# Kernel tuning notes

Measured on AMD Instinct MI355X. Metric: run time of the kernel, lower is better.

The kernel has to match this reference:

```python
import jax, jax.numpy as jnp
import numpy as np

B, K, D, L, POS = 128, 128, 512, 2, 64
DI = 2 * D           # d_inner = dim * expand(2)
HH, WW = 64, 64
GS = 16              # hilbert grid_size


def _ln(x, g, b):
    m = jnp.mean(x, axis=-1, keepdims=True)
    v = jnp.mean(jnp.square(x - m), axis=-1, keepdims=True)
    return (x - m) * jax.lax.rsqrt(v + 1e-5) * g + b


def _ssm(x, g, b, wi, bi, wo, bo):
    # LinearAttentionSSM: x + proj_out(silu(z) * sigmoid(gate)) with z,gate = proj_in(LN(x)).chunk(2)
    h = _ln(x, g, b) @ wi + bi
    z, gate = jnp.split(h, 2, axis=-1)
    return x + (jax.nn.silu(z) * jax.nn.sigmoid(gate)) @ wo + bo


def _hilbert_d(x, y, n=GS):
    # vectorized xy2d_hilbert over arbitrary int arrays
    d = jnp.zeros_like(x)
    s = n // 2
    while s > 0:
        rx = ((x & s) > 0).astype(jnp.int32)
        ry = ((y & s) > 0).astype(jnp.int32)
        d = d + s * s * jnp.bitwise_xor(3 * rx, ry)
        x, y = (jnp.where(ry == 0, jnp.where(rx == 1, s - 1 - y, y), x),
                jnp.where(ry == 0, jnp.where(rx == 1, s - 1 - x, x), y))
        s //= 2
    return d


def _forward(H, W, slots, keep_mask, attn_maps,
             pm1_w, pm1_b, pm2_w, pm2_b,
             fwd_ln_g, fwd_ln_b, fwd_in_w, fwd_in_b, fwd_out_w, fwd_out_b,
             bwd_ln_g, bwd_ln_b, bwd_in_w, bwd_in_b, bwd_out_w, bwd_out_b,
             merge_w, merge_b, norm_g, norm_b,
             ffn_ln_g, ffn_ln_b, ffn1_w, ffn1_b, ffn2_w, ffn2_b):
    Bz, Kz, Dz = slots.shape
    dt = slots.dtype
    # ---- SlotSpatialEncoder ----
    gy = jnp.arange(H, dtype=dt) / max(H - 1, 1)
    gx = jnp.arange(W, dtype=dt) / max(W - 1, 1)
    grid_y, grid_x = jnp.meshgrid(gy, gx, indexing='ij')
    coords = jnp.stack([grid_x.ravel(), grid_y.ravel()], axis=-1)       # [N,2]
    ap = attn_maps[:, :Kz, :]
    ap = ap / (ap.sum(axis=-1, keepdims=True) + 1e-8)
    centroids = jnp.einsum('bkn,nc->bkc', ap, coords)                   # [B,K,2]
    feats = jnp.concatenate([centroids, jnp.full_like(centroids, 0.1)], axis=-1)  # [B,K,4]
    freqs = 1.0 / (10000.0 ** (jnp.arange(0, POS, 2, dtype=jnp.float32) / POS))
    angles = feats[..., None] * freqs * 3.14159                         # [B,K,4,POS//2]
    enc = jnp.concatenate([jnp.sin(angles), jnp.cos(angles)], axis=-1).reshape(Bz, Kz, 4 * POS)
    pos_enc = jax.nn.gelu(enc @ pm1_w + pm1_b, approximate=False) @ pm2_w + pm2_b
    slots = slots + pos_enc
    # ---- Hilbert ordering (same centroids => same order each layer) ----
    cx = jnp.clip(centroids[..., 0] * (GS - 1), 0, GS - 1).astype(jnp.int32)
    cy = jnp.clip(centroids[..., 1] * (GS - 1), 0, GS - 1).astype(jnp.int32)
    order = jnp.argsort(_hilbert_d(cx, cy), axis=-1)                    # [B,K]
    reverse = jnp.argsort(order, axis=-1)
    # ---- layers ----
    for i in range(L):
        residual = slots
        ordered = jnp.take_along_axis(slots, order[..., None], axis=1)
        f = _ssm(ordered, fwd_ln_g[i], fwd_ln_b[i], fwd_in_w[i], fwd_in_b[i], fwd_out_w[i], fwd_out_b[i])
        bk = _ssm(ordered[:, ::-1], bwd_ln_g[i], bwd_ln_b[i], bwd_in_w[i], bwd_in_b[i], bwd_out_w[i], bwd_out_b[i])[:, ::-1]
        merged = jnp.concatenate([f, bk], axis=-1) @ merge_w[i] + merge_b[i]
        unord = jnp.take_along_axis(merged, reverse[..., None], axis=1)
        slots = _ln(residual + unord, norm_g[i], norm_b[i])
        ff = jax.nn.gelu(_ln(slots, ffn_ln_g[i], ffn_ln_b[i]) @ ffn1_w[i] + ffn1_b[i], approximate=False) @ ffn2_w[i] + ffn2_b[i]
        slots = slots + ff
        slots = slots * keep_mask[..., None]
    return slots, centroids


def setup_inputs() -> dict:
    key = jax.random.key(0)
    ks = iter(jax.random.split(key, 32))
    w = lambda *s: jax.random.normal(next(ks), s, jnp.float32) * 0.02
    z = lambda *s: jnp.zeros(s, jnp.float32)
    o = lambda *s: jnp.ones(s, jnp.float32)
    return {
        'slots': jax.random.normal(next(ks), (B, K, D), jnp.float32),
        'keep_mask': o(B, K),
        'attn_maps': jax.random.uniform(next(ks), (B, K, HH * WW), jnp.float32),
        'H': HH, 'W': WW,
        'pm1_w': w(4 * POS, D), 'pm1_b': z(D), 'pm2_w': w(D, D), 'pm2_b': z(D),
        'fwd_ln_g': o(L, D), 'fwd_ln_b': z(L, D),
        'fwd_in_w': w(L, D, 2 * DI), 'fwd_in_b': z(L, 2 * DI),
        'fwd_out_w': w(L, DI, D), 'fwd_out_b': z(L, D),
        'bwd_ln_g': o(L, D), 'bwd_ln_b': z(L, D),
        'bwd_in_w': w(L, D, 2 * DI), 'bwd_in_b': z(L, 2 * DI),
        'bwd_out_w': w(L, DI, D), 'bwd_out_b': z(L, D),
        'merge_w': w(L, 2 * D, D), 'merge_b': z(L, D),
        'norm_g': o(L, D), 'norm_b': z(L, D),
        'ffn_ln_g': o(L, D), 'ffn_ln_b': z(L, D),
        'ffn1_w': w(L, D, 4 * D), 'ffn1_b': z(L, 4 * D),
        'ffn2_w': w(L, 4 * D, D), 'ffn2_b': z(L, D),
    }


def reference(slots, keep_mask, attn_maps, H, W,
              pm1_w, pm1_b, pm2_w, pm2_b,
              fwd_ln_g, fwd_ln_b, fwd_in_w, fwd_in_b, fwd_out_w, fwd_out_b,
              bwd_ln_g, bwd_ln_b, bwd_in_w, bwd_in_b, bwd_out_w, bwd_out_b,
              merge_w, merge_b, norm_g, norm_b,
              ffn_ln_g, ffn_ln_b, ffn1_w, ffn1_b, ffn2_w, ffn2_b):
    return _forward(H, W, slots, keep_mask, attn_maps,
                    pm1_w, pm1_b, pm2_w, pm2_b,
                    fwd_ln_g, fwd_ln_b, fwd_in_w, fwd_in_b, fwd_out_w, fwd_out_b,
                    bwd_ln_g, bwd_ln_b, bwd_in_w, bwd_in_b, bwd_out_w, bwd_out_b,
                    merge_w, merge_b, norm_g, norm_b,
                    ffn_ln_g, ffn_ln_b, ffn1_w, ffn1_b, ffn2_w, ffn2_b)
```

## Files before the change

kernel.cpp:

```cpp
#include <hip/hip_runtime.h>

typedef __bf16 bf16_t;
typedef __bf16 bf16x8 __attribute__((ext_vector_type(8)));
typedef __bf16 bf16x4 __attribute__((ext_vector_type(4)));
typedef float  f32x4  __attribute__((ext_vector_type(4)));

#define MODE_GELU   0
#define MODE_GATED  1
#define MODE_RES_BF 2
#define MODE_RES_F  3
#define MODE_FFN2   4

__device__ __forceinline__ void async16(const void* g, void* l) {
  __builtin_amdgcn_global_load_lds(
      (const __attribute__((address_space(1))) void*)g,
      (__attribute__((address_space(3))) void*)l, 16, 0, 0);
}

__device__ __forceinline__ float fast_exp(float x) {
  return __builtin_amdgcn_exp2f(x * 1.44269504088896f);
}
__device__ __forceinline__ float fast_sigmoid(float x) {
  return __builtin_amdgcn_rcpf(1.0f + fast_exp(-x));
}
__device__ __forceinline__ float fast_gelu(float x) {
  float u = fabsf(x) * 0.70710678118f;
  float t = __builtin_amdgcn_rcpf(fmaf(0.3275911f, u, 1.0f));
  float p = t * fmaf(t, fmaf(t, fmaf(t, fmaf(t, 1.061405429f, -1.453152027f),
                                     1.421413741f), -0.284496736f), 0.254829592f);
  float e = __builtin_amdgcn_exp2f(-u * u * 1.44269504088896f);
  float erfu = fmaf(-p, e, 1.0f);
  float s = (x >= 0.f) ? erfu : -erfu;
  return 0.5f * x * (1.0f + s);
}

template<int MODE>
__launch_bounds__(256, 2)
__global__ void gemm_mfma(const bf16_t* __restrict__ A,
                          const bf16_t* __restrict__ B1,
                          const bf16_t* __restrict__ B2,
                          const float*  __restrict__ bias,
                          const float*  __restrict__ Xres,
                          const float*  __restrict__ mask,
                          void* __restrict__ Cptr,
                          int M, int N, int K, int ldC, int coff)
{
  constexpr bool DUAL = (MODE == MODE_GATED);
  __shared__ bf16_t sA[128 * 64];
  __shared__ bf16_t sB[128 * 64];
  __shared__ bf16_t sB2[DUAL ? 128 * 64 : 8];

  const int tid  = threadIdx.x;
  const int wave = tid >> 6;
  const int lane = tid & 63;
  const int wm = wave & 1;
  const int wn = wave >> 1;
  const long m0 = (long)blockIdx.y * 128;
  const long n0 = (long)blockIdx.x * 128;

  f32x4 zero4 = {0.f, 0.f, 0.f, 0.f};
  f32x4 acc[4][4];
  f32x4 acc2[DUAL ? 4 : 1][DUAL ? 4 : 1];
#pragma unroll
  for (int i = 0; i < 4; i++)
#pragma unroll
    for (int j = 0; j < 4; j++) acc[i][j] = zero4;
  if constexpr (DUAL) {
#pragma unroll
    for (int i = 0; i < 4; i++)
#pragma unroll
      for (int j = 0; j < 4; j++) acc2[i][j] = zero4;
  }

  const int q    = lane >> 4;
  const int c16  = lane & 15;
  const int sr   = lane >> 3;
  const int sg   = lane & 7;
  const int stRow = wave * 8 + sr;

  for (long k0 = 0; k0 < K; k0 += 64) {
#pragma unroll
    for (int i = 0; i < 4; i++) {
      int  r     = i * 32 + stRow;
      int  g     = sg ^ (r & 7);
      long goff  = (long)r * K + k0 + g * 8;
      int  lbase = i * 2048 + wave * 512;
      async16(A  + m0 * K + goff, &sA[lbase]);
      async16(B1 + n0 * K + goff, &sB[lbase]);
      if constexpr (DUAL) async16(B2 + n0 * K + goff, &sB2[lbase]);
    }
    __syncthreads();
#pragma unroll
    for (int kk = 0; kk < 2; kk++) {
      bf16x8 af[4], bfr[4], b2fr[DUAL ? 4 : 1];
#pragma unroll
      for (int i = 0; i < 4; i++) {
        int r = wm * 64 + i * 16 + c16;
        int g = (kk * 4 + q) ^ (r & 7);
        af[i] = *(const bf16x8*)&sA[r * 64 + g * 8];
      }
#pragma unroll
      for (int j = 0; j < 4; j++) {
        int r = wn * 64 + j * 16 + c16;
        int g = (kk * 4 + q) ^ (r & 7);
        bfr[j] = *(const bf16x8*)&sB[r * 64 + g * 8];
        if constexpr (DUAL) b2fr[j] = *(const bf16x8*)&sB2[r * 64 + g * 8];
      }
#pragma unroll
      for (int i = 0; i < 4; i++)
#pragma unroll
        for (int j = 0; j < 4; j++) {
          acc[i][j] = __builtin_amdgcn_mfma_f32_16x16x32_bf16(af[i], bfr[j], acc[i][j], 0, 0, 0);
          if constexpr (DUAL)
            acc2[i][j] = __builtin_amdgcn_mfma_f32_16x16x32_bf16(af[i], b2fr[j], acc2[i][j], 0, 0, 0);
        }
    }
    __syncthreads();
  }

#pragma unroll
  for (int i = 0; i < 4; i++) {
#pragma unroll
    for (int j = 0; j < 4; j++) {
#pragma unroll
      for (int r = 0; r < 4; r++) {
        long m = m0 + wm * 64 + i * 16 + q * 4 + r;
        long n = n0 + wn * 64 + j * 16 + c16;
        float v = acc[i][j][r];
        if constexpr (MODE == MODE_GELU) {
          float x  = v + bias[n];
          ((bf16_t*)Cptr)[m * (long)ldC + n] = (bf16_t)fast_gelu(x);
        } else if constexpr (MODE == MODE_GATED) {
          float z  = v + bias[n];
          float gt = acc2[i][j][r] + bias[N + n];
          float sz = z * fast_sigmoid(z);
          float sg_ = fast_sigmoid(gt);
          ((bf16_t*)Cptr)[m * (long)ldC + n] = (bf16_t)(sz * sg_);
        } else if constexpr (MODE == MODE_RES_BF) {
          float x = Xres[m * (long)N + n] + v + bias[n];
          ((bf16_t*)Cptr)[m * (long)ldC + coff + n] = (bf16_t)x;
        } else if constexpr (MODE == MODE_RES_F) {
          float x = Xres[m * (long)N + n] + v + bias[n];
          ((float*)Cptr)[m * (long)ldC + n] = x;
        } else {
          float x = (Xres[m * (long)N + n] + v + bias[n]) * mask[m];
          ((float*)Cptr)[m * (long)ldC + n] = x;
        }
      }
    }
  }
}

struct TransDesc { const float* src; bf16_t* dst; int K, N, tileBase; };
struct TransArgs { TransDesc d[16]; int nd; };

__global__ void transpose_all(TransArgs args) {
  __shared__ float tile[32][33];
  int bid = blockIdx.x;
  int di = 0;
  while (di + 1 < args.nd && bid >= args.d[di + 1].tileBase) ++di;
  TransDesc d = args.d[di];
  int t = bid - d.tileBase;
  int tilesX = d.N >> 5;
  int ty = t / tilesX, tx = t % tilesX;
  int lx = threadIdx.x & 31, ly = threadIdx.x >> 5;
  int gx = tx * 32 + lx;
#pragma unroll
  for (int i = 0; i < 32; i += 8) {
    int gy = ty * 32 + ly + i;
    tile[ly + i][lx] = d.src[(long)gy * d.N + gx];
  }
  __syncthreads();
  int ox = ty * 32 + lx;
#pragma unroll
  for (int i = 0; i < 32; i += 8) {
    int oy = tx * 32 + ly + i;
    d.dst[(long)oy * d.K + ox] = (bf16_t)tile[lx][ly + i];
  }
}

__global__ void centroid_kernel(const float* __restrict__ attn,
                                float* __restrict__ cent,
                                float* __restrict__ outCent) {
  int wave = threadIdx.x >> 6, lane = threadIdx.x & 63;
  long row = (long)blockIdx.x * 4 + wave;
  const float4* ap = (const float4*)(attn + row * 4096);
  float s = 0.f, sx = 0.f, sy = 0.f;
#pragma unroll 4
  for (int t = 0; t < 16; t++) {
    float4 v = ap[t * 64 + lane];
    int n0 = (t * 64 + lane) * 4;
    float col = (float)(n0 & 63);
    float ry  = (float)(n0 >> 6);
    float rs = v.x + v.y + v.z + v.w;
    s  += rs;
    sx += v.x * col + v.y * (col + 1.f) + v.z * (col + 2.f) + v.w * (col + 3.f);
    sy += rs * ry;
  }
#pragma unroll
  for (int o = 32; o; o >>= 1) {
    s += __shfl_down(s, o); sx += __shfl_down(sx, o); sy += __shfl_down(sy, o);
  }
  if (lane == 0) {
    float denom = s + 1e-8f;
    float cx = (sx * (1.f / 63.f)) / denom;
    float cy = (sy * (1.f / 63.f)) / denom;
    cent[row * 2] = cx;     cent[row * 2 + 1] = cy;
    outCent[row * 2] = cx;  outCent[row * 2 + 1] = cy;
  }
}

__global__ void enc_kernel(const float* __restrict__ cent, bf16_t* __restrict__ enc) {
  int tid = blockIdx.x * 256 + threadIdx.x;
  int row = tid >> 5, j = tid & 31;
  float cx = cent[row * 2], cy = cent[row * 2 + 1];
  float freq = expf(-(float)j * 0.28782313662425572f);
  float fx = cx * freq * 3.14159f;
  float fy = cy * freq * 3.14159f;
  float fc = 0.1f * freq * 3.14159f;
  bf16_t* e = enc + (long)row * 256;
  float sc = sinf(fc), cc = cosf(fc);
  e[j]        = (bf16_t)sinf(fx);  e[32 + j]  = (bf16_t)cosf(fx);
  e[64 + j]   = (bf16_t)sinf(fy);  e[96 + j]  = (bf16_t)cosf(fy);
  e[128 + j]  = (bf16_t)sc;        e[160 + j] = (bf16_t)cc;
  e[192 + j]  = (bf16_t)sc;        e[224 + j] = (bf16_t)cc;
}

__global__ void ln_in_kernel(const float* __restrict__ X,
                             const float* __restrict__ g1, const float* __restrict__ b1,
                             const float* __restrict__ g2, const float* __restrict__ b2,
                             bf16_t* __restrict__ O1, bf16_t* __restrict__ O2) {
  int wave = threadIdx.x >> 6, lane = threadIdx.x & 63;
  long row = (long)blockIdx.x * 4 + wave;
  const float4* xp = (const float4*)(X + row * 512);
  float4 v0 = xp[lane], v1 = xp[64 + lane];
  float s  = v0.x + v0.y + v0.z + v0.w + v1.x + v1.y + v1.z + v1.w;
  float s2 = v0.x*v0.x + v0.y*v0.y + v0.z*v0.z + v0.w*v0.w
           + v1.x*v1.x + v1.y*v1.y + v1.z*v1.z + v1.w*v1.w;
#pragma unroll
  for (int o = 32; o; o >>= 1) { s += __shfl_xor(s, o); s2 += __shfl_xor(s2, o); }
  float mean = s * (1.f / 512.f);
  float var  = s2 * (1.f / 512.f) - mean * mean;
  float rstd = rsqrtf(var + 1e-5f);
  float xs[8] = {v0.x, v0.y, v0.z, v0.w, v1.x, v1.y, v1.z, v1.w};
  int   c0 = lane * 4, c1 = 256 + lane * 4;
  bf16x4 pa, pb;
#pragma unroll
  for (int t = 0; t < 4; t++) {
    float nx = (xs[t] - mean) * rstd;
    pa[t] = (bf16_t)(nx * g1[c0 + t] + b1[c0 + t]);
    pb[t] = (bf16_t)(nx * g2[c0 + t] + b2[c0 + t]);
  }
  *(bf16x4*)&O1[row * 512 + c0] = pa;
  *(bf16x4*)&O2[row * 512 + c0] = pb;
#pragma unroll
  for (int t = 0; t < 4; t++) {
    float nx = (xs[4 + t] - mean) * rstd;
    pa[t] = (bf16_t)(nx * g1[c1 + t] + b1[c1 + t]);
    pb[t] = (bf16_t)(nx * g2[c1 + t] + b2[c1 + t]);
  }
  *(bf16x4*)&O1[row * 512 + c1] = pa;
  *(bf16x4*)&O2[row * 512 + c1] = pb;
}

__global__ void ln_dual_kernel(const float* __restrict__ U,
                               const float* __restrict__ ng, const float* __restrict__ nb,
                               const float* __restrict__ fg, const float* __restrict__ fb,
                               float* __restrict__ Y, bf16_t* __restrict__ Yln) {
  int wave = threadIdx.x >> 6, lane = threadIdx.x & 63;
  long row = (long)blockIdx.x * 4 + wave;
  const float4* xp = (const float4*)(U + row * 512);
  float4 v0 = xp[lane], v1 = xp[64 + lane];
  float s  = v0.x + v0.y + v0.z + v0.w + v1.x + v1.y + v1.z + v1.w;
  float s2 = v0.x*v0.x + v0.y*v0.y + v0.z*v0.z + v0.w*v0.w
           + v1.x*v1.x + v1.y*v1.y + v1.z*v1.z + v1.w*v1.w;
#pragma unroll
  for (int o = 32; o; o >>= 1) { s += __shfl_xor(s, o); s2 += __shfl_xor(s2, o); }
  float mean = s * (1.f / 512.f);
  float var  = s2 * (1.f / 512.f) - mean * mean;
  float rstd = rsqrtf(var + 1e-5f);
  float xs[8] = {v0.x, v0.y, v0.z, v0.w, v1.x, v1.y, v1.z, v1.w};
  int   c0 = lane * 4, c1 = 256 + lane * 4;
  float y[8];
#pragma unroll
  for (int t = 0; t < 4; t++) y[t]     = (xs[t] - mean) * rstd * ng[c0 + t] + nb[c0 + t];
#pragma unroll
  for (int t = 0; t < 4; t++) y[4 + t] = (xs[4 + t] - mean) * rstd * ng[c1 + t] + nb[c1 + t];
  float4 w0 = {y[0], y[1], y[2], y[3]}, w1 = {y[4], y[5], y[6], y[7]};
  float4* yp = (float4*)(Y + row * 512);
  yp[lane] = w0; yp[64 + lane] = w1;
  float t1 = 0.f, t2 = 0.f;
#pragma unroll
  for (int t = 0; t < 8; t++) { t1 += y[t]; t2 += y[t] * y[t]; }
#pragma unroll
  for (int o = 32; o; o >>= 1) { t1 += __shfl_xor(t1, o); t2 += __shfl_xor(t2, o); }
  float mean2 = t1 * (1.f / 512.f);
  float var2  = t2 * (1.f / 512.f) - mean2 * mean2;
  float rstd2 = rsqrtf(var2 + 1e-5f);
  bf16x4 pa;
#pragma unroll
  for (int t = 0; t < 4; t++) pa[t] = (bf16_t)((y[t] - mean2) * rstd2 * fg[c0 + t] + fb[c0 + t]);
  *(bf16x4*)&Yln[row * 512 + c0] = pa;
#pragma unroll
  for (int t = 0; t < 4; t++) pa[t] = (bf16_t)((y[4 + t] - mean2) * rstd2 * fg[c1 + t] + fb[c1 + t]);
  *(bf16x4*)&Yln[row * 512 + c1] = pa;
}

extern "C" void kernel_launch(void* const* d_in, const int* in_sizes, int n_in,
                              void* d_out, int out_size, void* d_ws, size_t ws_size,
                              hipStream_t stream) {
  const int M = 16384;
  const float* slots    = (const float*)d_in[0];
  const float* keep     = (const float*)d_in[1];
  const float* attn     = (const float*)d_in[2];
  const float* pm1_w    = (const float*)d_in[5];
  const float* pm1_b    = (const float*)d_in[6];
  const float* pm2_w    = (const float*)d_in[7];
  const float* pm2_b    = (const float*)d_in[8];
  const float* fwd_ln_g = (const float*)d_in[9];
  const float* fwd_ln_b = (const float*)d_in[10];
  const float* fwd_in_w = (const float*)d_in[11];
  const float* fwd_in_b = (const float*)d_in[12];
  const float* fwd_out_w= (const float*)d_in[13];
  const float* fwd_out_b= (const float*)d_in[14];
  const float* bwd_ln_g = (const float*)d_in[15];
  const float* bwd_ln_b = (const float*)d_in[16];
  const float* bwd_in_w = (const float*)d_in[17];
  const float* bwd_in_b = (const float*)d_in[18];
  const float* bwd_out_w= (const float*)d_in[19];
  const float* bwd_out_b= (const float*)d_in[20];
  const float* merge_w  = (const float*)d_in[21];
  const float* merge_b  = (const float*)d_in[22];
  const float* norm_g   = (const float*)d_in[23];
  const float* norm_b   = (const float*)d_in[24];
  const float* ffn_ln_g = (const float*)d_in[25];
  const float* ffn_ln_b = (const float*)d_in[26];
  const float* ffn1_w   = (const float*)d_in[27];
  const float* ffn1_b   = (const float*)d_in[28];
  const float* ffn2_w   = (const float*)d_in[29];
  const float* ffn2_b   = (const float*)d_in[30];

  char* w = (char*)d_ws;
  size_t off = 0;
  auto alloc = [&](size_t bytes) { size_t r = off; off += (bytes + 255) & ~(size_t)255; return r; };

  bf16_t* pm1t = (bf16_t*)(w + alloc(512 * 256 * 2));
  bf16_t* pm2t = (bf16_t*)(w + alloc(512 * 512 * 2));
  bf16_t *fwd_int[2], *fwd_outt[2], *bwd_int[2], *bwd_outt[2], *merget[2], *ffn1t[2], *ffn2t[2];
  for (int l = 0; l < 2; l++) {
    fwd_int[l]  = (bf16_t*)(w + alloc(2048 * 512 * 2));
    fwd_outt[l] = (bf16_t*)(w + alloc(512 * 1024 * 2));
    bwd_int[l]  = (bf16_t*)(w + alloc(2048 * 512 * 2));
    bwd_outt[l] = (bf16_t*)(w + alloc(512 * 1024 * 2));
    merget[l]   = (bf16_t*)(w + alloc(512 * 1024 * 2));
    ffn1t[l]    = (bf16_t*)(w + alloc(2048 * 512 * 2));
    ffn2t[l]    = (bf16_t*)(w + alloc(512 * 2048 * 2));
  }
  float* cent = (float*)(w + alloc((size_t)M * 2 * 4));
  float* X    = (float*)(w + alloc((size_t)M * 512 * 4));
  float* Y    = (float*)(w + alloc((size_t)M * 512 * 4));
  char* A1 = w + alloc((size_t)M * 2048 * 2);
  char* A2 = w + alloc((size_t)M * 2048 * 2);

  bf16_t* Enc = (bf16_t*)A1;
  bf16_t* P1  = (bf16_t*)A2;
  bf16_t* Xf  = (bf16_t*)A1;
  bf16_t* Xb  = (bf16_t*)(A1 + (size_t)M * 512 * 2);
  bf16_t* Gf  = (bf16_t*)A2;
  bf16_t* Gb  = (bf16_t*)(A2 + (size_t)M * 1024 * 2);
  bf16_t* FB  = (bf16_t*)A1;
  float*  U   = (float*)(A1 + (size_t)M * 1024 * 2);
  bf16_t* Yln = (bf16_t*)A2;
  bf16_t* FF1 = (bf16_t*)A1;

  TransArgs ta{};
  int nt = 0, tb = 0;
  auto addT = [&](const float* s, bf16_t* dst, int K, int N) {
    ta.d[nt].src = s; ta.d[nt].dst = dst; ta.d[nt].K = K; ta.d[nt].N = N; ta.d[nt].tileBase = tb;
    tb += (K * N) >> 10; nt++;
  };
  addT(pm1_w, pm1t, 256, 512);
  addT(pm2_w, pm2t, 512, 512);
  for (int l = 0; l < 2; l++) {
    addT(fwd_in_w  + (size_t)l * 512 * 2048, fwd_int[l],  512, 2048);
    addT(fwd_out_w + (size_t)l * 1024 * 512, fwd_outt[l], 1024, 512);
    addT(bwd_in_w  + (size_t)l * 512 * 2048, bwd_int[l],  512, 2048);
    addT(bwd_out_w + (size_t)l * 1024 * 512, bwd_outt[l], 1024, 512);
    addT(merge_w   + (size_t)l * 1024 * 512, merget[l],   1024, 512);
    addT(ffn1_w    + (size_t)l * 512 * 2048, ffn1t[l],    512, 2048);
    addT(ffn2_w    + (size_t)l * 2048 * 512, ffn2t[l],    2048, 512);
  }
  ta.nd = nt;
  transpose_all<<<tb, 256, 0, stream>>>(ta);

  float* outCent = (float*)d_out + (size_t)M * 512;
  centroid_kernel<<<M / 4, 256, 0, stream>>>(attn, cent, outCent);
  enc_kernel<<<(M * 32) / 256, 256, 0, stream>>>(cent, Enc);

  gemm_mfma<MODE_GELU><<<dim3(4, 128), 256, 0, stream>>>(
      Enc, pm1t, nullptr, pm1_b, nullptr, nullptr, P1, M, 512, 256, 512, 0);
  gemm_mfma<MODE_RES_F><<<dim3(4, 128), 256, 0, stream>>>(
      P1, pm2t, nullptr, pm2_b, slots, nullptr, X, M, 512, 512, 512, 0);

  for (int l = 0; l < 2; l++) {
    ln_in_kernel<<<M / 4, 256, 0, stream>>>(X,
        fwd_ln_g + l * 512, fwd_ln_b + l * 512,
        bwd_ln_g + l * 512, bwd_ln_b + l * 512, Xf, Xb);
    gemm_mfma<MODE_GATED><<<dim3(8, 128), 256, 0, stream>>>(
        Xf, fwd_int[l], fwd_int[l] + (size_t)1024 * 512, fwd_in_b + l * 2048,
        nullptr, nullptr, Gf, M, 1024, 512, 1024, 0);
    gemm_mfma<MODE_GATED><<<dim3(8, 128), 256, 0, stream>>>(
        Xb, bwd_int[l], bwd_int[l] + (size_t)1024 * 512, bwd_in_b + l * 2048,
        nullptr, nullptr, Gb, M, 1024, 512, 1024, 0);
    gemm_mfma<MODE_RES_BF><<<dim3(4, 128), 256, 0, stream>>>(
        Gf, fwd_outt[l], nullptr, fwd_out_b + l * 512, X, nullptr, FB, M, 512, 1024, 1024, 0);
    gemm_mfma<MODE_RES_BF><<<dim3(4, 128), 256, 0, stream>>>(
        Gb, bwd_outt[l], nullptr, bwd_out_b + l * 512, X, nullptr, FB, M, 512, 1024, 1024, 512);
    gemm_mfma<MODE_RES_F><<<dim3(4, 128), 256, 0, stream>>>(
        FB, merget[l], nullptr, merge_b + l * 512, X, nullptr, U, M, 512, 1024, 512, 0);
    ln_dual_kernel<<<M / 4, 256, 0, stream>>>(U,
        norm_g + l * 512, norm_b + l * 512,
        ffn_ln_g + l * 512, ffn_ln_b + l * 512, Y, Yln);
    gemm_mfma<MODE_GELU><<<dim3(16, 128), 256, 0, stream>>>(
        Yln, ffn1t[l], nullptr, ffn1_b + l * 2048, nullptr, nullptr, FF1, M, 2048, 512, 2048, 0);
    float* Xdst = (l == 1) ? (float*)d_out : X;
    gemm_mfma<MODE_FFN2><<<dim3(4, 128), 256, 0, stream>>>(
        FF1, ffn2t[l], nullptr, ffn2_b + l * 512, Y, keep, Xdst, M, 512, 2048, 512, 0);
  }
}
```

Measured before the change: 1.118 ms.

## Fold LN affine and out/merge projections into precomputed composite weights

Folds the LayerNorm gamma/beta into the input-projection weights and biases, so a single plain normalization feeds both the forward and backward gated GEMMs, now merged into one launch. The out-projection and merge weights are pre-multiplied into a composite matrix, with the residual term x·(Mf+Mb) appended, so one K=2560 GEMM replaces the two out-projection GEMMs and the merge GEMM. This removes intermediate activation traffic and several launches. In exchange it adds setup kernels for the weight products and GEMV-based bias folding, changes bf16 rounding order, and raises launch bounds on the non-gated GEMMs.

```diff
diff --git a/kernel.cpp b/kernel.cpp
--- a/kernel.cpp
+++ b/kernel.cpp
@@ -7,9 +7,9 @@
 
 #define MODE_GELU   0
 #define MODE_GATED  1
-#define MODE_RES_BF 2
 #define MODE_RES_F  3
 #define MODE_FFN2   4
+#define MODE_STORE  5
 
 __device__ __forceinline__ void async16(const void* g, void* l) {
   __builtin_amdgcn_global_load_lds(
@@ -35,7 +35,7 @@
 }
 
 template<int MODE>
-__launch_bounds__(256, 2)
+__launch_bounds__(256, (MODE == MODE_GATED) ? 2 : 3)
 __global__ void gemm_mfma(const bf16_t* __restrict__ A,
                           const bf16_t* __restrict__ B1,
                           const bf16_t* __restrict__ B2,
@@ -43,7 +43,7 @@
                           const float*  __restrict__ Xres,
                           const float*  __restrict__ mask,
                           void* __restrict__ Cptr,
-                          int M, int N, int K, int ldC, int coff)
+                          int M, int N, int K, int lda, int ldC, int coff)
 {
   constexpr bool DUAL = (MODE == MODE_GATED);
   __shared__ bf16_t sA[128 * 64];
@@ -83,11 +83,12 @@
     for (int i = 0; i < 4; i++) {
       int  r     = i * 32 + stRow;
       int  g     = sg ^ (r & 7);
-      long goff  = (long)r * K + k0 + g * 8;
+      long gA    = (long)r * lda + k0 + g * 8;
+      long gB    = (long)r * K   + k0 + g * 8;
       int  lbase = i * 2048 + wave * 512;
-      async16(A  + m0 * K + goff, &sA[lbase]);
-      async16(B1 + n0 * K + goff, &sB[lbase]);
-      if constexpr (DUAL) async16(B2 + n0 * K + goff, &sB2[lbase]);
+      async16(A  + m0 * lda + gA, &sA[lbase]);
+      async16(B1 + n0 * K   + gB, &sB[lbase]);
+      if constexpr (DUAL) async16(B2 + n0 * K + gB, &sB2[lbase]);
     }
     __syncthreads();
 #pragma unroll
@@ -136,23 +137,23 @@
           float sz = z * fast_sigmoid(z);
           float sg_ = fast_sigmoid(gt);
           ((bf16_t*)Cptr)[m * (long)ldC + n] = (bf16_t)(sz * sg_);
-        } else if constexpr (MODE == MODE_RES_BF) {
-          float x = Xres[m * (long)N + n] + v + bias[n];
-          ((bf16_t*)Cptr)[m * (long)ldC + coff + n] = (bf16_t)x;
         } else if constexpr (MODE == MODE_RES_F) {
           float x = Xres[m * (long)N + n] + v + bias[n];
           ((float*)Cptr)[m * (long)ldC + n] = x;
-        } else {
+        } else if constexpr (MODE == MODE_FFN2) {
           float x = (Xres[m * (long)N + n] + v + bias[n]) * mask[m];
           ((float*)Cptr)[m * (long)ldC + n] = x;
+        } else {
+          ((bf16_t*)Cptr)[m * (long)ldC + coff + n] = (bf16_t)v;
         }
       }
     }
   }
 }
 
-struct TransDesc { const float* src; bf16_t* dst; int K, N, tileBase; };
-struct TransArgs { TransDesc d[16]; int nd; };
+struct TransDesc { const float* src; bf16_t* dst; const float* rowScale;
+                   int K, ncols, srcLd, srcColOff, tileBase, mode; };
+struct TransArgs { TransDesc d[24]; int nd; };
 
 __global__ void transpose_all(TransArgs args) {
   __shared__ float tile[32][33];
@@ -161,14 +162,22 @@
   while (di + 1 < args.nd && bid >= args.d[di + 1].tileBase) ++di;
   TransDesc d = args.d[di];
   int t = bid - d.tileBase;
-  int tilesX = d.N >> 5;
+  if (d.mode == 1) {
+    long idx = (long)t * 1024 + threadIdx.x * 4;
+    float4 v = *(const float4*)(d.src + idx);
+    bf16x4 o; o[0] = (bf16_t)v.x; o[1] = (bf16_t)v.y; o[2] = (bf16_t)v.z; o[3] = (bf16_t)v.w;
+    *(bf16x4*)(d.dst + idx) = o;
+    return;
+  }
+  int tilesX = d.ncols >> 5;
   int ty = t / tilesX, tx = t % tilesX;
   int lx = threadIdx.x & 31, ly = threadIdx.x >> 5;
   int gx = tx * 32 + lx;
 #pragma unroll
   for (int i = 0; i < 32; i += 8) {
     int gy = ty * 32 + ly + i;
-    tile[ly + i][lx] = d.src[(long)gy * d.N + gx];
+    float sc = d.rowScale ? d.rowScale[gy] : 1.f;
+    tile[ly + i][lx] = d.src[(long)gy * d.srcLd + d.srcColOff + gx] * sc;
   }
   __syncthreads();
   int ox = ty * 32 + lx;
@@ -177,6 +186,44 @@
     int oy = tx * 32 + ly + i;
     d.dst[(long)oy * d.K + ox] = (bf16_t)tile[lx][ly + i];
   }
+}
+
+struct GemvDesc { const float* v; const float* W; const float* b0; float* out;
+                  int K, ldW, colOff, jBase, N; };
+struct GemvArgs { GemvDesc d[12]; int nd; };
+
+__global__ void gemv_all(GemvArgs a) {
+  int j = blockIdx.x * 256 + threadIdx.x;
+  int di = 0;
+  while (di + 1 < a.nd && j >= a.d[di + 1].jBase) ++di;
+  GemvDesc d = a.d[di];
+  int jj = j - d.jBase;
+  if (jj >= d.N) return;
+  float s = d.b0 ? d.b0[jj] : 0.f;
+  for (int k = 0; k < d.K; k++) s += d.v[k] * d.W[(long)k * d.ldW + d.colOff + jj];
+  d.out[jj] = s;
+}
+
+__global__ void bias_u_kernel(const float* __restrict__ fob, const float* __restrict__ bob,
+                              const float* __restrict__ mw, const float* __restrict__ mb,
+                              float* __restrict__ out) {
+  int n = blockIdx.x * 256 + threadIdx.x;
+  float s = mb[n];
+  for (int k = 0; k < 512; k++)
+    s += fob[k] * mw[k * 512 + n] + bob[k] * mw[(512 + k) * 512 + n];
+  out[n] = s;
+}
+
+__global__ void build_mtmb(const bf16_t* __restrict__ mt0, bf16_t* __restrict__ bc0,
+                           const bf16_t* __restrict__ mt1, bf16_t* __restrict__ bc1) {
+  int idx = blockIdx.x * 256 + threadIdx.x;
+  int l = idx >> 18;
+  int r = idx & 262143;
+  int n = r >> 9, k = r & 511;
+  const bf16_t* mt = l ? mt1 : mt0;
+  bf16_t* bc = l ? bc1 : bc0;
+  float v = (float)mt[n * 1024 + k] + (float)mt[n * 1024 + 512 + k];
+  bc[(long)n * 2560 + 2048 + k] = (bf16_t)v;
 }
 
 __global__ void centroid_kernel(const float* __restrict__ attn,
@@ -226,10 +273,8 @@
   e[192 + j]  = (bf16_t)sc;        e[224 + j] = (bf16_t)cc;
 }
 
-__global__ void ln_in_kernel(const float* __restrict__ X,
-                             const float* __restrict__ g1, const float* __restrict__ b1,
-                             const float* __restrict__ g2, const float* __restrict__ b2,
-                             bf16_t* __restrict__ O1, bf16_t* __restrict__ O2) {
+__global__ void ln_plain_kernel(const float* __restrict__ X,
+                                bf16_t* __restrict__ Xn, bf16_t* __restrict__ Sx) {
   int wave = threadIdx.x >> 6, lane = threadIdx.x & 63;
   long row = (long)blockIdx.x * 4 + wave;
   const float4* xp = (const float4*)(X + row * 512);
@@ -244,28 +289,25 @@
   float rstd = rsqrtf(var + 1e-5f);
   float xs[8] = {v0.x, v0.y, v0.z, v0.w, v1.x, v1.y, v1.z, v1.w};
   int   c0 = lane * 4, c1 = 256 + lane * 4;
-  bf16x4 pa, pb;
+  bf16x4 pa, pr;
 #pragma unroll
   for (int t = 0; t < 4; t++) {
-    float nx = (xs[t] - mean) * rstd;
-    pa[t] = (bf16_t)(nx * g1[c0 + t] + b1[c0 + t]);
-    pb[t] = (bf16_t)(nx * g2[c0 + t] + b2[c0 + t]);
-  }
-  *(bf16x4*)&O1[row * 512 + c0] = pa;
-  *(bf16x4*)&O2[row * 512 + c0] = pb;
+    pa[t] = (bf16_t)((xs[t] - mean) * rstd);
+    pr[t] = (bf16_t)xs[t];
+  }
+  *(bf16x4*)&Xn[row * 512 + c0] = pa;
+  *(bf16x4*)&Sx[row * 2560 + c0] = pr;
 #pragma unroll
   for (int t = 0; t < 4; t++) {
-    float nx = (xs[4 + t] - mean) * rstd;
-    pa[t] = (bf16_t)(nx * g1[c1 + t] + b1[c1 + t]);
-    pb[t] = (bf16_t)(nx * g2[c1 + t] + b2[c1 + t]);
-  }
-  *(bf16x4*)&O1[row * 512 + c1] = pa;
-  *(bf16x4*)&O2[row * 512 + c1] = pb;
+    pa[t] = (bf16_t)((xs[4 + t] - mean) * rstd);
+    pr[t] = (bf16_t)xs[4 + t];
+  }
+  *(bf16x4*)&Xn[row * 512 + c1] = pa;
+  *(bf16x4*)&Sx[row * 2560 + c1] = pr;
 }
 
 __global__ void ln_dual_kernel(const float* __restrict__ U,
                                const float* __restrict__ ng, const float* __restrict__ nb,
-                               const float* __restrict__ fg, const float* __restrict__ fb,
                                float* __restrict__ Y, bf16_t* __restrict__ Yln) {
   int wave = threadIdx.x >> 6, lane = threadIdx.x & 63;
   long row = (long)blockIdx.x * 4 + wave;
@@ -299,10 +341,10 @@
   float rstd2 = rsqrtf(var2 + 1e-5f);
   bf16x4 pa;
 #pragma unroll
-  for (int t = 0; t < 4; t++) pa[t] = (bf16_t)((y[t] - mean2) * rstd2 * fg[c0 + t] + fb[c0 + t]);
+  for (int t = 0; t < 4; t++) pa[t] = (bf16_t)((y[t] - mean2) * rstd2);
   *(bf16x4*)&Yln[row * 512 + c0] = pa;
 #pragma unroll
-  for (int t = 0; t < 4; t++) pa[t] = (bf16_t)((y[4 + t] - mean2) * rstd2 * fg[c1 + t] + fb[c1 + t]);
+  for (int t = 0; t < 4; t++) pa[t] = (bf16_t)((y[4 + t] - mean2) * rstd2);
   *(bf16x4*)&Yln[row * 512 + c1] = pa;
 }
 
@@ -346,85 +388,116 @@
 
   bf16_t* pm1t = (bf16_t*)(w + alloc(512 * 256 * 2));
   bf16_t* pm2t = (bf16_t*)(w + alloc(512 * 512 * 2));
-  bf16_t *fwd_int[2], *fwd_outt[2], *bwd_int[2], *bwd_outt[2], *merget[2], *ffn1t[2], *ffn2t[2];
+  bf16_t *WzT[2], *WgT[2], *ffn1t[2], *ffn2t[2], *merget[2], *foutbf[2], *boutbf[2], *Bcomp[2];
+  float  *bias_gated[2], *bias_ffn1[2], *bias_u[2];
   for (int l = 0; l < 2; l++) {
-    fwd_int[l]  = (bf16_t*)(w + alloc(2048 * 512 * 2));
-    fwd_outt[l] = (bf16_t*)(w + alloc(512 * 1024 * 2));
-    bwd_int[l]  = (bf16_t*)(w + alloc(2048 * 512 * 2));
-    bwd_outt[l] = (bf16_t*)(w + alloc(512 * 1024 * 2));
-    merget[l]   = (bf16_t*)(w + alloc(512 * 1024 * 2));
-    ffn1t[l]    = (bf16_t*)(w + alloc(2048 * 512 * 2));
-    ffn2t[l]    = (bf16_t*)(w + alloc(512 * 2048 * 2));
-  }
-  float* cent = (float*)(w + alloc((size_t)M * 2 * 4));
-  float* X    = (float*)(w + alloc((size_t)M * 512 * 4));
-  float* Y    = (float*)(w + alloc((size_t)M * 512 * 4));
-  char* A1 = w + alloc((size_t)M * 2048 * 2);
-  char* A2 = w + alloc((size_t)M * 2048 * 2);
-
-  bf16_t* Enc = (bf16_t*)A1;
-  bf16_t* P1  = (bf16_t*)A2;
-  bf16_t* Xf  = (bf16_t*)A1;
-  bf16_t* Xb  = (bf16_t*)(A1 + (size_t)M * 512 * 2);
-  bf16_t* Gf  = (bf16_t*)A2;
-  bf16_t* Gb  = (bf16_t*)(A2 + (size_t)M * 1024 * 2);
-  bf16_t* FB  = (bf16_t*)A1;
-  float*  U   = (float*)(A1 + (size_t)M * 1024 * 2);
-  bf16_t* Yln = (bf16_t*)A2;
-  bf16_t* FF1 = (bf16_t*)A1;
+    WzT[l]    = (bf16_t*)(w + alloc(2048 * 512 * 2));
+    WgT[l]    = (bf16_t*)(w + alloc(2048 * 512 * 2));
+    ffn1t[l]  = (bf16_t*)(w + alloc(2048 * 512 * 2));
+    ffn2t[l]  = (bf16_t*)(w + alloc(512 * 2048 * 2));
+    merget[l] = (bf16_t*)(w + alloc(512 * 1024 * 2));
+    foutbf[l] = (bf16_t*)(w + alloc(1024 * 512 * 2));
+    boutbf[l] = (bf16_t*)(w + alloc(1024 * 512 * 2));
+    Bcomp[l]  = (bf16_t*)(w + alloc(512 * 2560 * 2));
+    bias_gated[l] = (float*)(w + alloc(4096 * 4));
+    bias_ffn1[l]  = (float*)(w + alloc(2048 * 4));
+    bias_u[l]     = (float*)(w + alloc(512 * 4));
+  }
+  float*  cent = (float*)(w + alloc((size_t)M * 2 * 4));
+  float*  X    = (float*)(w + alloc((size_t)M * 512 * 4));
+  float*  Y    = (float*)(w + alloc((size_t)M * 512 * 4));
+  float*  U    = (float*)(w + alloc((size_t)M * 512 * 4));
+  bf16_t* Xn   = (bf16_t*)(w + alloc((size_t)M * 512 * 2));
+  bf16_t* S    = (bf16_t*)(w + alloc((size_t)M * 2560 * 2));
+  bf16_t* FF1  = (bf16_t*)(w + alloc((size_t)M * 2048 * 2));
+  bf16_t* Yln  = (bf16_t*)(w + alloc((size_t)M * 512 * 2));
+  bf16_t* Enc  = (bf16_t*)(w + alloc((size_t)M * 256 * 2));
+  bf16_t* P1   = (bf16_t*)(w + alloc((size_t)M * 512 * 2));
+
+  const size_t WSTRIDE = (size_t)512 * 2048;
 
   TransArgs ta{};
   int nt = 0, tb = 0;
-  auto addT = [&](const float* s, bf16_t* dst, int K, int N) {
-    ta.d[nt].src = s; ta.d[nt].dst = dst; ta.d[nt].K = K; ta.d[nt].N = N; ta.d[nt].tileBase = tb;
-    tb += (K * N) >> 10; nt++;
+  auto addT = [&](const float* s, bf16_t* dst, const float* scale,
+                  int K, int ncols, int srcLd, int srcColOff, int mode) {
+    ta.d[nt] = {s, dst, scale, K, ncols, srcLd, srcColOff, tb, mode};
+    tb += (K * ncols) >> 10; nt++;
   };
-  addT(pm1_w, pm1t, 256, 512);
-  addT(pm2_w, pm2t, 512, 512);
+  addT(pm1_w, pm1t, nullptr, 256, 512, 512, 0, 0);
+  addT(pm2_w, pm2t, nullptr, 512, 512, 512, 0, 0);
   for (int l = 0; l < 2; l++) {
-    addT(fwd_in_w  + (size_t)l * 512 * 2048, fwd_int[l],  512, 2048);
-    addT(fwd_out_w + (size_t)l * 1024 * 512, fwd_outt[l], 1024, 512);
-    addT(bwd_in_w  + (size_t)l * 512 * 2048, bwd_int[l],  512, 2048);
-    addT(bwd_out_w + (size_t)l * 1024 * 512, bwd_outt[l], 1024, 512);
-    addT(merge_w   + (size_t)l * 1024 * 512, merget[l],   1024, 512);
-    addT(ffn1_w    + (size_t)l * 512 * 2048, ffn1t[l],    512, 2048);
-    addT(ffn2_w    + (size_t)l * 2048 * 512, ffn2t[l],    2048, 512);
+    const float* fiw = fwd_in_w + (size_t)l * WSTRIDE;
+    const float* biw = bwd_in_w + (size_t)l * WSTRIDE;
+    addT(fiw, WzT[l],               fwd_ln_g + l * 512, 512, 1024, 2048, 0,    0);
+    addT(biw, WzT[l] + 1024 * 512,  bwd_ln_g + l * 512, 512, 1024, 2048, 0,    0);
+    addT(fiw, WgT[l],               fwd_ln_g + l * 512, 512, 1024, 2048, 1024, 0);
+    addT(biw, WgT[l] + 1024 * 512,  bwd_ln_g + l * 512, 512, 1024, 2048, 1024, 0);
+    addT(merge_w + (size_t)l * 1024 * 512, merget[l], nullptr, 1024, 512, 512, 0, 0);
+    addT(ffn1_w + (size_t)l * WSTRIDE, ffn1t[l], ffn_ln_g + l * 512, 512, 2048, 2048, 0, 0);
+    addT(ffn2_w + (size_t)l * WSTRIDE, ffn2t[l], nullptr, 2048, 512, 512, 0, 0);
+    addT(fwd_out_w + (size_t)l * 1024 * 512, foutbf[l], nullptr, 1024, 512, 0, 0, 1);
+    addT(bwd_out_w + (size_t)l * 1024 * 512, boutbf[l], nullptr, 1024, 512, 0, 0, 1);
   }
   ta.nd = nt;
   transpose_all<<<tb, 256, 0, stream>>>(ta);
+
+  for (int l = 0; l < 2; l++) {
+    gemm_mfma<MODE_STORE><<<dim3(8, 4), 256, 0, stream>>>(
+        merget[l], foutbf[l], nullptr, nullptr, nullptr, nullptr,
+        Bcomp[l], 512, 1024, 512, 1024, 2560, 0);
+    gemm_mfma<MODE_STORE><<<dim3(8, 4), 256, 0, stream>>>(
+        merget[l] + 512, boutbf[l], nullptr, nullptr, nullptr, nullptr,
+        Bcomp[l], 512, 1024, 512, 1024, 2560, 1024);
+  }
+  build_mtmb<<<2048, 256, 0, stream>>>(merget[0], Bcomp[0], merget[1], Bcomp[1]);
+
+  GemvArgs ga{};
+  int ng_ = 0, jb = 0;
+  auto addG = [&](const float* v, const float* W, const float* b0, float* out,
+                  int K, int ldW, int colOff, int N) {
+    ga.d[ng_] = {v, W, b0, out, K, ldW, colOff, jb, N};
+    jb += N; ng_++;
+  };
+  for (int l = 0; l < 2; l++) {
+    const float* fiw = fwd_in_w + (size_t)l * WSTRIDE;
+    const float* biw = bwd_in_w + (size_t)l * WSTRIDE;
+    addG(fwd_ln_b + l * 512, fiw, fwd_in_b + l * 2048,        bias_gated[l],        512, 2048, 0,    1024);
+    addG(bwd_ln_b + l * 512, biw, bwd_in_b + l * 2048,        bias_gated[l] + 1024, 512, 2048, 0,    1024);
+    addG(fwd_ln_b + l * 512, fiw, fwd_in_b + l * 2048 + 1024, bias_gated[l] + 2048, 512, 2048, 1024, 1024);
+    addG(bwd_ln_b + l * 512, biw, bwd_in_b + l * 2048 + 1024, bias_gated[l] + 3072, 512, 2048, 1024, 1024);
+    addG(ffn_ln_b + l * 512, ffn1_w + (size_t)l * WSTRIDE, ffn1_b + l * 2048, bias_ffn1[l], 512, 2048, 0, 2048);
+  }
+  ga.nd = ng_;
+  gemv_all<<<jb / 256, 256, 0, stream>>>(ga);
+  for (int l = 0; l < 2; l++)
+    bias_u_kernel<<<2, 256, 0, stream>>>(fwd_out_b + l * 512, bwd_out_b + l * 512,
+                                         merge_w + (size_t)l * 1024 * 512,
+                                         merge_b + l * 512, bias_u[l]);
 
   float* outCent = (float*)d_out + (size_t)M * 512;
   centroid_kernel<<<M / 4, 256, 0, stream>>>(attn, cent, outCent);
   enc_kernel<<<(M * 32) / 256, 256, 0, stream>>>(cent, Enc);
 
   gemm_mfma<MODE_GELU><<<dim3(4, 128), 256, 0, stream>>>(
-      Enc, pm1t, nullptr, pm1_b, nullptr, nullptr, P1, M, 512, 256, 512, 0);
+      Enc, pm1t, nullptr, pm1_b, nullptr, nullptr, P1, M, 512, 256, 256, 512, 0);
   gemm_mfma<MODE_RES_F><<<dim3(4, 128), 256, 0, stream>>>(
-      P1, pm2t, nullptr, pm2_b, slots, nullptr, X, M, 512, 512, 512, 0);
+      P1, pm2t, nullptr, pm2_b, slots, nullptr, X, M, 512, 512, 512, 512, 0);
 
   for (int l = 0; l < 2; l++) {
-    ln_in_kernel<<<M / 4, 256, 0, stream>>>(X,
-        fwd_ln_g + l * 512, fwd_ln_b + l * 512,
-        bwd_ln_g + l * 512, bwd_ln_b + l * 512, Xf, Xb);
-    gemm_mfma<MODE_GATED><<<dim3(8, 128), 256, 0, stream>>>(
-        Xf, fwd_int[l], fwd_int[l] + (size_t)1024 * 512, fwd_in_b + l * 2048,
-        nullptr, nullptr, Gf, M, 1024, 512, 1024, 0);
-    gemm_mfma<MODE_GATED><<<dim3(8, 128), 256, 0, stream>>>(
-        Xb, bwd_int[l], bwd_int[l] + (size_t)1024 * 512, bwd_in_b + l * 2048,
-        nullptr, nullptr, Gb, M, 1024, 512, 1024, 0);
-    gemm_mfma<MODE_RES_BF><<<dim3(4, 128), 256, 0, stream>>>(
-        Gf, fwd_outt[l], nullptr, fwd_out_b + l * 512, X, nullptr, FB, M, 512, 1024, 1024, 0);
-    gemm_mfma<MODE_RES_BF><<<dim3(4, 128), 256, 0, stream>>>(
-        Gb, bwd_outt[l], nullptr, bwd_out_b + l * 512, X, nullptr, FB, M, 512, 1024, 1024, 512);
+    ln_plain_kernel<<<M / 4, 256, 0, stream>>>(X, Xn, S + 2048);
+    gemm_mfma<MODE_GATED><<<dim3(16, 128), 256, 0, stream>>>(
+        Xn, WzT[l], WgT[l], bias_gated[l], nullptr, nullptr, S,
+        M, 2048, 512, 512, 2560, 0);
     gemm_mfma<MODE_RES_F><<<dim3(4, 128), 256, 0, stream>>>(
-        FB, merget[l], nullptr, merge_b + l * 512, X, nullptr, U, M, 512, 1024, 512, 0);
-    ln_dual_kernel<<<M / 4, 256, 0, stream>>>(U,
-        norm_g + l * 512, norm_b + l * 512,
-        ffn_ln_g + l * 512, ffn_ln_b + l * 512, Y, Yln);
+        S, Bcomp[l], nullptr, bias_u[l], X, nullptr, U,
+        M, 512, 2560, 2560, 512, 0);
+    ln_dual_kernel<<<M / 4, 256, 0, stream>>>(U, norm_g + l * 512, norm_b + l * 512, Y, Yln);
     gemm_mfma<MODE_GELU><<<dim3(16, 128), 256, 0, stream>>>(
-        Yln, ffn1t[l], nullptr, ffn1_b + l * 2048, nullptr, nullptr, FF1, M, 2048, 512, 2048, 0);
+        Yln, ffn1t[l], nullptr, bias_ffn1[l], nullptr, nullptr, FF1,
+        M, 2048, 512, 512, 2048, 0);
     float* Xdst = (l == 1) ? (float*)d_out : X;
     gemm_mfma<MODE_FFN2><<<dim3(4, 128), 256, 0, stream>>>(
-        FF1, ffn2t[l], nullptr, ffn2_b + l * 512, Y, keep, Xdst, M, 512, 2048, 512, 0);
-  }
-}
+        FF1, ffn2t[l], nullptr, ffn2_b + l * 512, Y, keep, Xdst,
+        M, 512, 2048, 2048, 512, 0);
+  }
+}
```

Result: slower. 1.315 ms (+17.6%).
